# Performance work log

Hardware: AMD Instinct MI355X
Metric: run time of the kernel (lower is better)

## Reference

```python
import jax, jax.numpy as jnp
import numpy as np

# Scaled-down LLaMA-style decoder with per-layer memory K/V prefix (tokenmix2 Decoder)
L, D, H, Dh, F, V = 2, 4096, 32, 128, 8192, 8192
B, S, M = 1, 1024, 512
EPS = 1e-5
ROPE_BASE = 10000.0


def setup_inputs() -> dict:
    key = jax.random.key(0)
    ks = jax.random.split(key, 16)
    sd = D ** -0.5
    sf = F ** -0.5
    n = lambda k, shape, s: (jax.random.normal(k, shape, jnp.float32) * s)
    return {
        "input_ids": jax.random.randint(ks[0], (B, S), 0, V),
        "memory": jax.random.normal(ks[1], (L, B, M, D), jnp.float32),
        "embed": n(ks[2], (V, D), sd),
        "Wq": n(ks[3], (L, D, D), sd),
        "Wk": n(ks[4], (L, D, D), sd),
        "Wv": n(ks[5], (L, D, D), sd),
        "Wo": n(ks[6], (L, D, D), sd),
        "Wg": n(ks[7], (L, F, D), sd),
        "Wu": n(ks[8], (L, F, D), sd),
        "Wd": n(ks[9], (L, D, F), sf),
        "Wmk": n(ks[10], (L, D, D), sd),
        "Wmv": n(ks[11], (L, D, D), sd),
        "ln1": jnp.ones((L, D), jnp.float32),
        "ln2": jnp.ones((L, D), jnp.float32),
        "normw": jnp.ones((D,), jnp.float32),
        "lm_head": n(ks[12], (V, D), sd),
    }


def _rms(x, w):
    return x * jax.lax.rsqrt(jnp.mean(x * x, axis=-1, keepdims=True) + EPS) * w


def _rot_half(x):
    x1, x2 = jnp.split(x, 2, axis=-1)
    return jnp.concatenate([-x2, x1], axis=-1)


def _rope_tables(n_pos):
    inv_freq = 1.0 / (ROPE_BASE ** (jnp.arange(0, Dh, 2, dtype=jnp.float32) / Dh))
    ang = jnp.arange(n_pos, dtype=jnp.float32)[:, None] * inv_freq[None, :]
    emb = jnp.concatenate([ang, ang], axis=-1)  # [n_pos, Dh]
    return jnp.cos(emb), jnp.sin(emb)


def reference(input_ids, memory, embed, Wq, Wk, Wv, Wo, Wg, Wu, Wd, Wmk, Wmv,
              ln1, ln2, normw, lm_head):
    h = embed[input_ids]                                   # [B,S,D]
    cos, sin = _rope_tables(M + S)                         # memory tokens sit at positions 0..M
    cos_k, sin_k = cos[None, None], sin[None, None]        # [1,1,M+S,Dh]
    cos_q, sin_q = cos[None, None, M:], sin[None, None, M:]  # queries at positions M..M+S
    qpos = jnp.arange(M, M + S)
    kpos = jnp.arange(M + S)
    mask = qpos[:, None] >= kpos[None, :]                  # causal incl. full memory prefix
    scale = Dh ** -0.5

    def heads(x, T):
        return x.reshape(B, T, H, Dh).transpose(0, 2, 1, 3)  # [B,H,T,Dh]

    for l in range(L):
        x = _rms(h, ln1[l])
        q = heads(x @ Wq[l].T, S)
        k = heads(x @ Wk[l].T, S)
        v = heads(x @ Wv[l].T, S)
        mk = heads(memory[l] @ Wmk[l].T, M)
        mv = heads(memory[l] @ Wmv[l].T, M)
        K = jnp.concatenate([mk, k], axis=2)               # [B,H,M+S,Dh]
        Vv = jnp.concatenate([mv, v], axis=2)
        q = q * cos_q + _rot_half(q) * sin_q
        K = K * cos_k + _rot_half(K) * sin_k
        scores = jnp.einsum('bhqd,bhkd->bhqk', q, K) * scale
        scores = jnp.where(mask, scores, jnp.float32(-1e30))
        p = jax.nn.softmax(scores, axis=-1)
        o = jnp.einsum('bhqk,bhkd->bhqd', p, Vv)
        o = o.transpose(0, 2, 1, 3).reshape(B, S, D)
        h = h + o @ Wo[l].T
        x = _rms(h, ln2[l])
        h = h + (jax.nn.silu(x @ Wg[l].T) * (x @ Wu[l].T)) @ Wd[l].T

    h = _rms(h, normw)
    logits = (h @ lm_head.T).astype(jnp.float32)           # [B,S,V]
    return logits
```

## Files before the change

kernel.cpp:

```cpp
#include <hip/hip_runtime.h>
#include <hip/hip_bf16.h>

typedef unsigned int uint;
typedef unsigned short u16;

#define D_ 4096
#define H_ 32
#define DH 128
#define F_ 8192
#define V_ 8192
#define S_ 1024
#define M_ 512
#define L_ 2
#define KV_ (M_ + S_)

typedef __attribute__((ext_vector_type(8))) short s16x8;
typedef __attribute__((ext_vector_type(4))) float f32x4;
typedef __attribute__((ext_vector_type(4))) u16 u16x4;

__device__ __forceinline__ u16 f2bf(float f) {
    uint u = __float_as_uint(f);
    u += 0x7FFFu + ((u >> 16) & 1u);
    return (u16)(u >> 16);
}
__device__ __forceinline__ float bf2f(u16 h) {
    return __uint_as_float(((uint)h) << 16);
}
__device__ __forceinline__ void gload_lds16(const void* g, void* l) {
    __builtin_amdgcn_global_load_lds(
        (const __attribute__((address_space(1))) unsigned int*)g,
        (__attribute__((address_space(3))) unsigned int*)l, 16, 0, 0);
}

__global__ void k_embed(const int* __restrict__ ids, const float* __restrict__ embed,
                        float* __restrict__ h) {
    int row = blockIdx.x;
    const float4* src = (const float4*)(embed + (size_t)ids[row] * D_);
    float4* dst = (float4*)(h + (size_t)row * D_);
    for (int i = threadIdx.x; i < D_ / 4; i += 256) dst[i] = src[i];
}

__global__ __launch_bounds__(256) void k_rms(const float* __restrict__ hin,
                                             const float* __restrict__ w,
                                             u16* __restrict__ out) {
    int row = blockIdx.x, t = threadIdx.x;
    const float4* src = (const float4*)(hin + (size_t)row * D_);
    float4 v[4];
    float ss = 0.f;
#pragma unroll
    for (int i = 0; i < 4; ++i) {
        v[i] = src[t + 256 * i];
        ss += v[i].x * v[i].x + v[i].y * v[i].y + v[i].z * v[i].z + v[i].w * v[i].w;
    }
#pragma unroll
    for (int off = 32; off; off >>= 1) ss += __shfl_xor(ss, off);
    __shared__ float red[4];
    if ((t & 63) == 0) red[t >> 6] = ss;
    __syncthreads();
    float tot = red[0] + red[1] + red[2] + red[3];
    float sc = rsqrtf(tot * (1.0f / D_) + 1e-5f);
    const float4* wp = (const float4*)w;
    u16x4* op = (u16x4*)(out + (size_t)row * D_);
#pragma unroll
    for (int i = 0; i < 4; ++i) {
        float4 wv = wp[t + 256 * i];
        u16x4 o;
        o[0] = f2bf(v[i].x * sc * wv.x);
        o[1] = f2bf(v[i].y * sc * wv.y);
        o[2] = f2bf(v[i].z * sc * wv.z);
        o[3] = f2bf(v[i].w * sc * wv.w);
        op[t + 256 * i] = o;
    }
}

__global__ void k_cvt(const float* __restrict__ src, u16* __restrict__ dst, int n4) {
    int i = blockIdx.x * 256 + threadIdx.x;
    if (i < n4) {
        float4 v = ((const float4*)src)[i];
        u16x4 o;
        o[0] = f2bf(v.x); o[1] = f2bf(v.y); o[2] = f2bf(v.z); o[3] = f2bf(v.w);
        ((u16x4*)dst)[i] = o;
    }
}

__global__ void k_silu(const float* __restrict__ G, const float* __restrict__ U,
                       u16* __restrict__ out, int n4) {
    int i = blockIdx.x * 256 + threadIdx.x;
    if (i < n4) {
        float4 g = ((const float4*)G)[i];
        float4 u = ((const float4*)U)[i];
        u16x4 o;
        o[0] = f2bf(g.x / (1.0f + __expf(-g.x)) * u.x);
        o[1] = f2bf(g.y / (1.0f + __expf(-g.y)) * u.y);
        o[2] = f2bf(g.z / (1.0f + __expf(-g.z)) * u.z);
        o[3] = f2bf(g.w / (1.0f + __expf(-g.w)) * u.w);
        ((u16x4*)out)[i] = o;
    }
}

__global__ void k_ropetab(float* __restrict__ tab) {
    int pos = blockIdx.x, i = threadIdx.x;
    float invf = powf(10000.0f, -(float)i * (1.0f / 64.0f));
    float ang = (float)pos * invf;
    tab[(size_t)pos * 128 + i * 2] = cosf(ang);
    tab[(size_t)pos * 128 + i * 2 + 1] = sinf(ang);
}

__global__ __launch_bounds__(256) void k_rope(u16* __restrict__ buf,
                                              const float* __restrict__ tab, int pos0) {
    int row = blockIdx.x, t = threadIdx.x;
    const float2* tp = (const float2*)(tab + (size_t)(pos0 + row) * 128);
    u16* p = buf + (size_t)row * D_;
#pragma unroll
    for (int j = 0; j < 8; ++j) {
        int pid = t + 256 * j;
        int hd = pid >> 6, i = pid & 63;
        float2 cs = tp[i];
        int base = hd * 128 + i;
        float v0 = bf2f(p[base]), v1 = bf2f(p[base + 64]);
        p[base] = f2bf(v0 * cs.x - v1 * cs.y);
        p[base + 64] = f2bf(v1 * cs.x + v0 * cs.y);
    }
}

__global__ __launch_bounds__(256) void k_transpose(const u16* __restrict__ src,
                                                   u16* __restrict__ dst) {
    __shared__ u16 tile[64][66];
    int tc = blockIdx.x * 64;
    int tr = blockIdx.y * 64;
    int t = threadIdx.x;
    int c = t & 63, r0 = t >> 6;
#pragma unroll
    for (int i = 0; i < 16; ++i) {
        int r = r0 + i * 4;
        tile[r][c] = src[(size_t)(tr + r) * D_ + tc + c];
    }
    __syncthreads();
#pragma unroll
    for (int i = 0; i < 16; ++i) {
        int r = r0 + i * 4;
        dst[(size_t)(tc + r) * KV_ + tr + c] = tile[c][r];
    }
}

struct GemmB8 {
    const u16* A[5];
    const u16* B[5];
    void* O[5];
    int mrows[5];
};

template <int EPI>
__global__ __launch_bounds__(512, 2) void k_gemm8(GemmB8 P, int Nn, int Kfull) {
    int z = blockIdx.z;
    size_t bm = blockIdx.y, bn = blockIdx.x;
    if ((int)(bm * 256) >= P.mrows[z]) return;
    const u16* A = P.A[z];
    const u16* Bw = P.B[z];
    __shared__ __align__(16) u16 AB[2][2][2][128][64];

    const int tid = threadIdx.x;
    const int lane = tid & 63, wid = tid >> 6;
    const int l16 = lane & 15, lh = lane >> 4;
    const int wrow = (wid >> 2) * 64;
    const int wcol = (wid & 3) * 32;
    const int nt = Kfull >> 6;

    const int grow0 = tid >> 3;
    const int gsw = ((tid & 7) ^ (grow0 & 7)) * 8;
    const u16* pA = A + (size_t)(bm * 256 + grow0) * Kfull + gsw;
    const u16* pB = Bw + (size_t)(bn * 256 + grow0) * Kfull + gsw;

    auto stage = [&](const u16* base, int mat, int h, int t) {
        if (t >= nt) return;
        const u16* g = base + (size_t)(h * 128) * Kfull + t * 64;
        u16* l = &AB[t & 1][mat][h][0][0] + tid * 8;
        gload_lds16(g, l);
        gload_lds16(g + (size_t)64 * Kfull, l + 4096);
    };

    f32x4 acc[4][4][2];
#pragma unroll
    for (int q = 0; q < 4; ++q)
#pragma unroll
        for (int mf = 0; mf < 4; ++mf)
#pragma unroll
            for (int nf = 0; nf < 2; ++nf)
#pragma unroll
                for (int e = 0; e < 4; ++e) acc[q][mf][nf][e] = 0.f;

    stage(pA, 0, 0, 0); stage(pB, 1, 0, 0);
    stage(pA, 0, 1, 0); stage(pB, 1, 1, 0);
    stage(pA, 0, 0, 1); stage(pB, 1, 0, 1);
    asm volatile("s_waitcnt vmcnt(4)" ::: "memory");
    __builtin_amdgcn_s_barrier();
    asm volatile("" ::: "memory");

    for (int T = 0; T < nt; ++T) {
        const int cb = T & 1;
#pragma unroll
        for (int q = 0; q < 4; ++q) {
            const int qm = q >> 1, qn = q & 1;
            s16x8 af[4][2], bb[2][2];
#pragma unroll
            for (int kk = 0; kk < 2; ++kk) {
                const int g0 = kk * 4 + lh;
                const int sw = (g0 ^ (l16 & 7)) * 8;
#pragma unroll
                for (int mf = 0; mf < 4; ++mf)
                    af[mf][kk] = *(const s16x8*)(&AB[cb][0][qm][wrow + mf * 16 + l16][sw]);
#pragma unroll
                for (int nf = 0; nf < 2; ++nf)
                    bb[nf][kk] = *(const s16x8*)(&AB[cb][1][qn][wcol + nf * 16 + l16][sw]);
            }
            if (q == 0) stage(pA, 0, 1, T + 1);
            else if (q == 1) stage(pB, 1, 1, T + 1);
            else if (q == 2) stage(pA, 0, 0, T + 2);
            else stage(pB, 1, 0, T + 2);
            asm volatile("" ::: "memory");
            __builtin_amdgcn_s_barrier();
            asm volatile("" ::: "memory");
            __builtin_amdgcn_s_setprio(1);
#pragma unroll
            for (int kk = 0; kk < 2; ++kk)
#pragma unroll
                for (int mf = 0; mf < 4; ++mf)
#pragma unroll
                    for (int nf = 0; nf < 2; ++nf)
                        acc[q][mf][nf] = __builtin_amdgcn_mfma_f32_16x16x32_bf16(
                            af[mf][kk], bb[nf][kk], acc[q][mf][nf], 0, 0, 0);
            __builtin_amdgcn_s_setprio(0);
            if (q == 3) {
                if (T < nt - 2) asm volatile("s_waitcnt vmcnt(4)" ::: "memory");
                else if (T == nt - 2) asm volatile("s_waitcnt vmcnt(0)" ::: "memory");
            }
            asm volatile("" ::: "memory");
            __builtin_amdgcn_s_barrier();
            asm volatile("" ::: "memory");
        }
    }

    void* Oo = P.O[z];
#pragma unroll
    for (int q = 0; q < 4; ++q) {
        const int qm = q >> 1, qn = q & 1;
#pragma unroll
        for (int mf = 0; mf < 4; ++mf) {
#pragma unroll
            for (int nf = 0; nf < 2; ++nf) {
#pragma unroll
                for (int rr = 0; rr < 4; ++rr) {
                    int grow = (int)bm * 256 + qm * 128 + wrow + mf * 16 + lh * 4 + rr;
                    int gcol = (int)bn * 256 + qn * 128 + wcol + nf * 16 + l16;
                    size_t idx = (size_t)grow * Nn + gcol;
                    float v = acc[q][mf][nf][rr];
                    if constexpr (EPI == 0) ((u16*)Oo)[idx] = f2bf(v);
                    else ((float*)Oo)[idx] = v;
                }
            }
        }
    }
}

struct GemmB2 {
    const u16* A[5];
    const u16* B[5];
    void* O[5];
    int mrows[5];
};

template <int EPI>
__global__ __launch_bounds__(256) void k_gemm2(GemmB2 P, int Nn, int Kfull) {
    int z = blockIdx.z;
    size_t bm = blockIdx.y, bn = blockIdx.x;
    if ((int)(bm * 128) >= P.mrows[z]) return;
    const u16* A = P.A[z];
    const u16* Bw = P.B[z];
    __shared__ __align__(16) u16 As[128 * 64];
    __shared__ __align__(16) u16 Bs[128 * 64];
    int tid = threadIdx.x;
    int lane = tid & 63, wid = tid >> 6;
    int l16 = lane & 15, lh = lane >> 4;
    int wm = (wid >> 1) * 64, wn = (wid & 1) * 64;

    const u16 *pA[4], *pB[4];
    int ldso[4];
#pragma unroll
    for (int i = 0; i < 4; ++i) {
        int c = tid + 256 * i;
        int r = c >> 3, s = c & 7;
        int ssw = (s ^ (r & 7)) * 8;
        pA[i] = A + (size_t)(bm * 128 + r) * Kfull + ssw;
        pB[i] = Bw + (size_t)(bn * 128 + r) * Kfull + ssw;
        ldso[i] = c * 8;
    }

    f32x4 acc[4][4];
#pragma unroll
    for (int i = 0; i < 4; ++i)
#pragma unroll
        for (int j = 0; j < 4; ++j)
#pragma unroll
            for (int e = 0; e < 4; ++e) acc[i][j][e] = 0.f;

    int nt = Kfull >> 6;
    for (int t = 0; t < nt; ++t) {
        int k0 = t << 6;
#pragma unroll
        for (int i = 0; i < 4; ++i) gload_lds16(pA[i] + k0, &As[ldso[i]]);
#pragma unroll
        for (int i = 0; i < 4; ++i) gload_lds16(pB[i] + k0, &Bs[ldso[i]]);
        __syncthreads();
#pragma unroll
        for (int kk = 0; kk < 2; ++kk) {
            int sidx = kk * 4 + lh;
            int sw = (sidx ^ (l16 & 7)) * 8;
            s16x8 af[4], bf4[4];
#pragma unroll
            for (int mi = 0; mi < 4; ++mi)
                af[mi] = *(const s16x8*)(&As[(wm + mi * 16 + l16) * 64 + sw]);
#pragma unroll
            for (int ni = 0; ni < 4; ++ni)
                bf4[ni] = *(const s16x8*)(&Bs[(wn + ni * 16 + l16) * 64 + sw]);
#pragma unroll
            for (int mi = 0; mi < 4; ++mi)
#pragma unroll
                for (int ni = 0; ni < 4; ++ni)
                    acc[mi][ni] = __builtin_amdgcn_mfma_f32_16x16x32_bf16(
                        af[mi], bf4[ni], acc[mi][ni], 0, 0, 0);
        }
        __syncthreads();
    }

    void* Oo = P.O[z];
#pragma unroll
    for (int mi = 0; mi < 4; ++mi) {
#pragma unroll
        for (int ni = 0; ni < 4; ++ni) {
#pragma unroll
            for (int r = 0; r < 4; ++r) {
                int grow = (int)bm * 128 + wm + mi * 16 + lh * 4 + r;
                int gcol = (int)bn * 128 + wn + ni * 16 + l16;
                size_t idx = (size_t)grow * Nn + gcol;
                float v = acc[mi][ni][r];
                if constexpr (EPI == 1) ((float*)Oo)[idx] = v;
                else ((float*)Oo)[idx] += v;
            }
        }
    }
}

__global__ __launch_bounds__(64) void k_attn(const u16* __restrict__ Qb,
                                             const u16* __restrict__ Kb,
                                             const u16* __restrict__ VT,
                                             u16* __restrict__ Ob) {
    int qt = blockIdx.x, hd = blockIdx.y;
    int lane = threadIdx.x, l16 = lane & 15, lh = lane >> 4;
    __shared__ __align__(16) float Pl[16 * 36];

    s16x8 qf[4];
#pragma unroll
    for (int c = 0; c < 4; ++c)
        qf[c] = *(const s16x8*)(Qb + (size_t)(qt * 16 + l16) * D_ + hd * DH + c * 32 + lh * 8);

    f32x4 o[8];
#pragma unroll
    for (int dc = 0; dc < 8; ++dc)
#pragma unroll
        for (int e = 0; e < 4; ++e) o[dc][e] = 0.f;
    float m[4], lsum[4];
#pragma unroll
    for (int r = 0; r < 4; ++r) { m[r] = -1e30f; lsum[r] = 0.f; }

    const float scale = 0.08838834764831845f;
    int qbase = M_ + qt * 16;
    int nkb = (M_ + qt * 16 + 16 + 31) >> 5;

    for (int kb = 0; kb < nkb; ++kb) {
        f32x4 s0, s1;
#pragma unroll
        for (int e = 0; e < 4; ++e) { s0[e] = 0.f; s1[e] = 0.f; }
#pragma unroll
        for (int c = 0; c < 4; ++c) {
            s16x8 kf0 = *(const s16x8*)(Kb + (size_t)(kb * 32 + l16) * D_ + hd * DH + c * 32 + lh * 8);
            s16x8 kf1 = *(const s16x8*)(Kb + (size_t)(kb * 32 + 16 + l16) * D_ + hd * DH + c * 32 + lh * 8);
            s0 = __builtin_amdgcn_mfma_f32_16x16x32_bf16(qf[c], kf0, s0, 0, 0, 0);
            s1 = __builtin_amdgcn_mfma_f32_16x16x32_bf16(qf[c], kf1, s1, 0, 0, 0);
        }
        int kp0 = kb * 32 + l16, kp1 = kp0 + 16;
        float pm[4];
#pragma unroll
        for (int r = 0; r < 4; ++r) {
            int qp = qbase + lh * 4 + r;
            float v0 = s0[r] * scale; if (kp0 > qp) v0 = -1e30f;
            float v1 = s1[r] * scale; if (kp1 > qp) v1 = -1e30f;
            s0[r] = v0; s1[r] = v1;
            pm[r] = fmaxf(v0, v1);
        }
#pragma unroll
        for (int r = 0; r < 4; ++r) {
#pragma unroll
            for (int off = 8; off; off >>= 1) pm[r] = fmaxf(pm[r], __shfl_xor(pm[r], off));
        }
        float alpha[4];
#pragma unroll
        for (int r = 0; r < 4; ++r) {
            float mn = fmaxf(m[r], pm[r]);
            alpha[r] = __expf(m[r] - mn);
            m[r] = mn;
            float p0 = __expf(s0[r] - mn), p1 = __expf(s1[r] - mn);
            s0[r] = p0; s1[r] = p1;
            float t = p0 + p1;
#pragma unroll
            for (int off = 8; off; off >>= 1) t += __shfl_xor(t, off);
            lsum[r] = lsum[r] * alpha[r] + t;
        }
#pragma unroll
        for (int r = 0; r < 4; ++r) {
            Pl[(lh * 4 + r) * 36 + l16] = s0[r];
            Pl[(lh * 4 + r) * 36 + 16 + l16] = s1[r];
        }
        __syncthreads();
        s16x8 pf;
        {
            const f32x4* pp = (const f32x4*)(Pl + l16 * 36 + lh * 8);
            f32x4 a = pp[0], b = pp[1];
            pf[0] = (short)f2bf(a[0]); pf[1] = (short)f2bf(a[1]);
            pf[2] = (short)f2bf(a[2]); pf[3] = (short)f2bf(a[3]);
            pf[4] = (short)f2bf(b[0]); pf[5] = (short)f2bf(b[1]);
            pf[6] = (short)f2bf(b[2]); pf[7] = (short)f2bf(b[3]);
        }
        __syncthreads();
#pragma unroll
        for (int dc = 0; dc < 8; ++dc) {
#pragma unroll
            for (int r = 0; r < 4; ++r) o[dc][r] *= alpha[r];
        }
#pragma unroll
        for (int dc = 0; dc < 8; ++dc) {
            s16x8 vf = *(const s16x8*)(VT + (size_t)(hd * DH + dc * 16 + l16) * KV_ + kb * 32 + lh * 8);
            o[dc] = __builtin_amdgcn_mfma_f32_16x16x32_bf16(pf, vf, o[dc], 0, 0, 0);
        }
    }
#pragma unroll
    for (int dc = 0; dc < 8; ++dc) {
#pragma unroll
        for (int r = 0; r < 4; ++r) {
            float val = o[dc][r] / lsum[r];
            Ob[(size_t)(qt * 16 + lh * 4 + r) * D_ + hd * DH + dc * 16 + l16] = f2bf(val);
        }
    }
}

extern "C" void kernel_launch(void* const* d_in, const int* in_sizes, int n_in,
                              void* d_out, int out_size, void* d_ws, size_t ws_size,
                              hipStream_t stream) {
    const int* ids = (const int*)d_in[0];
    const float* memory = (const float*)d_in[1];
    const float* embed = (const float*)d_in[2];
    const float* Wq = (const float*)d_in[3];
    const float* Wk = (const float*)d_in[4];
    const float* Wv = (const float*)d_in[5];
    const float* Wo = (const float*)d_in[6];
    const float* Wg = (const float*)d_in[7];
    const float* Wu = (const float*)d_in[8];
    const float* Wd = (const float*)d_in[9];
    const float* Wmk = (const float*)d_in[10];
    const float* Wmv = (const float*)d_in[11];
    const float* ln1 = (const float*)d_in[12];
    const float* ln2 = (const float*)d_in[13];
    const float* normw = (const float*)d_in[14];
    const float* lm = (const float*)d_in[15];

    char* ws = (char*)d_ws;
    float* h   = (float*)(ws + 0x0000000);
    u16* xb    = (u16*)(ws + 0x1000000);
    float* tab = (float*)(ws + 0x1800000);
    u16* memb  = (u16*)(ws + 0x1900000);
    u16* Qb    = (u16*)(ws + 0x1E00000);
    u16* Kb    = (u16*)(ws + 0x2600000);
    u16* Vb    = (u16*)(ws + 0x3200000);
    u16* VT    = (u16*)(ws + 0x3E00000);
    u16* Ob    = (u16*)(ws + 0x4A00000);
    float* Gbuf = (float*)(ws + 0x1E00000);
    u16* tb     = (u16*)(ws + 0x3E00000);
    float* Ubuf = (float*)(ws + 0x4E00000);
    u16* Wqb  = (u16*)(ws + 0x07000000);
    u16* Wkb  = (u16*)(ws + 0x0B000000);
    u16* Wvb  = (u16*)(ws + 0x0F000000);
    u16* Wob  = (u16*)(ws + 0x13000000);
    u16* Wmkb = (u16*)(ws + 0x17000000);
    u16* Wmvb = (u16*)(ws + 0x1B000000);
    u16* Wgb  = (u16*)(ws + 0x1F000000);
    u16* Wub  = (u16*)(ws + 0x27000000);
    u16* Wdb  = (u16*)(ws + 0x2F000000);
    u16* lmb  = (u16*)(ws + 0x37000000);

    const int nDD = L_ * D_ * D_ / 4, nFD = L_ * F_ * D_ / 4, nVD = V_ * D_ / 4;
    k_cvt<<<(nDD + 255) / 256, 256, 0, stream>>>(Wq, Wqb, nDD);
    k_cvt<<<(nDD + 255) / 256, 256, 0, stream>>>(Wk, Wkb, nDD);
    k_cvt<<<(nDD + 255) / 256, 256, 0, stream>>>(Wv, Wvb, nDD);
    k_cvt<<<(nDD + 255) / 256, 256, 0, stream>>>(Wo, Wob, nDD);
    k_cvt<<<(nDD + 255) / 256, 256, 0, stream>>>(Wmk, Wmkb, nDD);
    k_cvt<<<(nDD + 255) / 256, 256, 0, stream>>>(Wmv, Wmvb, nDD);
    k_cvt<<<(nFD + 255) / 256, 256, 0, stream>>>(Wg, Wgb, nFD);
    k_cvt<<<(nFD + 255) / 256, 256, 0, stream>>>(Wu, Wub, nFD);
    k_cvt<<<(nFD + 255) / 256, 256, 0, stream>>>(Wd, Wdb, nFD);
    k_cvt<<<(nVD + 255) / 256, 256, 0, stream>>>(lm, lmb, nVD);

    k_embed<<<S_, 256, 0, stream>>>(ids, embed, h);
    k_ropetab<<<KV_, 64, 0, stream>>>(tab);

    for (int l = 0; l < L_; ++l) {
        const size_t oDD = (size_t)l * D_ * D_;
        const size_t oFD = (size_t)l * F_ * D_;

        k_rms<<<S_, 256, 0, stream>>>(h, ln1 + l * D_, xb);
        k_cvt<<<(M_ * D_ / 4 + 255) / 256, 256, 0, stream>>>(
            memory + (size_t)l * M_ * D_, memb, M_ * D_ / 4);

        GemmB8 g1{};
        g1.A[0] = xb;   g1.B[0] = Wqb + oDD;  g1.O[0] = Qb;                    g1.mrows[0] = S_;
        g1.A[1] = xb;   g1.B[1] = Wkb + oDD;  g1.O[1] = Kb + (size_t)M_ * D_;  g1.mrows[1] = S_;
        g1.A[2] = xb;   g1.B[2] = Wvb + oDD;  g1.O[2] = Vb + (size_t)M_ * D_;  g1.mrows[2] = S_;
        g1.A[3] = memb; g1.B[3] = Wmkb + oDD; g1.O[3] = Kb;                    g1.mrows[3] = M_;
        g1.A[4] = memb; g1.B[4] = Wmvb + oDD; g1.O[4] = Vb;                    g1.mrows[4] = M_;
        k_gemm8<0><<<dim3(D_ / 256, S_ / 256, 5), 512, 0, stream>>>(g1, D_, D_);

        k_rope<<<S_, 256, 0, stream>>>(Qb, tab, M_);
        k_rope<<<KV_, 256, 0, stream>>>(Kb, tab, 0);
        k_transpose<<<dim3(D_ / 64, KV_ / 64), 256, 0, stream>>>(Vb, VT);
        k_attn<<<dim3(S_ / 16, H_), 64, 0, stream>>>(Qb, Kb, VT, Ob);

        GemmB2 g2{};
        g2.A[0] = Ob; g2.B[0] = Wob + oDD; g2.O[0] = h; g2.mrows[0] = S_;
        k_gemm2<2><<<dim3(D_ / 128, S_ / 128, 1), 256, 0, stream>>>(g2, D_, D_);

        k_rms<<<S_, 256, 0, stream>>>(h, ln2 + l * D_, xb);
        GemmB8 g3{};
        g3.A[0] = xb; g3.B[0] = Wgb + oFD; g3.O[0] = Gbuf; g3.mrows[0] = S_;
        g3.A[1] = xb; g3.B[1] = Wub + oFD; g3.O[1] = Ubuf; g3.mrows[1] = S_;
        k_gemm8<1><<<dim3(F_ / 256, S_ / 256, 2), 512, 0, stream>>>(g3, F_, D_);
        k_silu<<<(S_ * F_ / 4 + 255) / 256, 256, 0, stream>>>(Gbuf, Ubuf, tb, S_ * F_ / 4);
        GemmB2 g5{};
        g5.A[0] = tb; g5.B[0] = Wdb + oFD; g5.O[0] = h; g5.mrows[0] = S_;
        k_gemm2<2><<<dim3(D_ / 128, S_ / 128, 1), 256, 0, stream>>>(g5, D_, F_);
    }

    k_rms<<<S_, 256, 0, stream>>>(h, normw, xb);
    GemmB2 g6{};
    g6.A[0] = xb; g6.B[0] = lmb; g6.O[0] = (float*)d_out; g6.mrows[0] = S_;
    k_gemm2<1><<<dim3(V_ / 128, S_ / 128, 1), 256, 0, stream>>>(g6, V_, D_);
}
```

Measured before the change: 2.155 ms.

## Fuse fp32-to-bf16 weight conversion into GEMM B-operand loading

Drops the separate conversion kernels that turned every fp32 weight matrix into bf16 in the workspace before each run. The GEMM kernels now read fp32 weights directly into registers, convert them with packed bf16 instructions and write them swizzled into LDS, with the prefetch schedule and wait counts reworked. This removes a full read and write pass over roughly a gigabyte of weights. In exchange the GEMMs read twice the bytes for B, and register-staged loads replace the asynchronous direct-to-LDS path, which can hurt latency hiding. Gate and up GEMM tiles are reused across 4 row blocks, so they re-read fp32 several times.

After: 1.955 ms. 9.3% less time.

```diff
diff --git a/kernel.cpp b/kernel.cpp
--- a/kernel.cpp
+++ b/kernel.cpp
@@ -25,6 +25,11 @@
 }
 __device__ __forceinline__ float bf2f(u16 h) {
     return __uint_as_float(((uint)h) << 16);
+}
+__device__ __forceinline__ uint cvt_pk_bf16(float a, float b) {
+    uint r;
+    asm volatile("v_cvt_pk_bf16_f32 %0, %1, %2" : "=v"(r) : "v"(a), "v"(b));
+    return r;
 }
 __device__ __forceinline__ void gload_lds16(const void* g, void* l) {
     __builtin_amdgcn_global_load_lds(
@@ -145,7 +150,7 @@
 
 struct GemmB8 {
     const u16* A[5];
-    const u16* B[5];
+    const float* B[5];
     void* O[5];
     int mrows[5];
 };
@@ -156,7 +161,7 @@
     size_t bm = blockIdx.y, bn = blockIdx.x;
     if ((int)(bm * 256) >= P.mrows[z]) return;
     const u16* A = P.A[z];
-    const u16* Bw = P.B[z];
+    const float* Bw = P.B[z];
     __shared__ __align__(16) u16 AB[2][2][2][128][64];
 
     const int tid = threadIdx.x;
@@ -169,16 +174,38 @@
     const int grow0 = tid >> 3;
     const int gsw = ((tid & 7) ^ (grow0 & 7)) * 8;
     const u16* pA = A + (size_t)(bm * 256 + grow0) * Kfull + gsw;
-    const u16* pB = Bw + (size_t)(bn * 256 + grow0) * Kfull + gsw;
-
-    auto stage = [&](const u16* base, int mat, int h, int t) {
+    auto stageA = [&](int h, int t) {
         if (t >= nt) return;
-        const u16* g = base + (size_t)(h * 128) * Kfull + t * 64;
-        u16* l = &AB[t & 1][mat][h][0][0] + tid * 8;
+        const u16* g = pA + (size_t)(h * 128) * Kfull + t * 64;
+        u16* l = &AB[t & 1][0][h][0][0] + tid * 8;
         gload_lds16(g, l);
         gload_lds16(g + (size_t)64 * Kfull, l + 4096);
     };
 
+    const int brow = tid >> 3;
+    const int bg = tid & 7;
+    const float* pB = Bw + (size_t)(bn * 256 + brow) * Kfull + bg * 8;
+    const int bwo = ((bg ^ (brow & 7)) * 8);
+    auto loadB = [&](int h, int t, float4* br) {
+        if (t >= nt) return;
+        const float* g = pB + (size_t)(h * 128) * Kfull + t * 64;
+        br[0] = *(const float4*)g;
+        br[1] = *(const float4*)(g + 4);
+        const float* g2 = g + (size_t)64 * Kfull;
+        br[2] = *(const float4*)g2;
+        br[3] = *(const float4*)(g2 + 4);
+    };
+    auto writeB = [&](int h, int t, const float4* br) {
+        if (t >= nt) return;
+        uint4 w0, w1;
+        w0.x = cvt_pk_bf16(br[0].x, br[0].y); w0.y = cvt_pk_bf16(br[0].z, br[0].w);
+        w0.z = cvt_pk_bf16(br[1].x, br[1].y); w0.w = cvt_pk_bf16(br[1].z, br[1].w);
+        w1.x = cvt_pk_bf16(br[2].x, br[2].y); w1.y = cvt_pk_bf16(br[2].z, br[2].w);
+        w1.z = cvt_pk_bf16(br[3].x, br[3].y); w1.w = cvt_pk_bf16(br[3].z, br[3].w);
+        *(uint4*)(&AB[t & 1][1][h][brow][bwo]) = w0;
+        *(uint4*)(&AB[t & 1][1][h][brow + 64][bwo]) = w1;
+    };
+
     f32x4 acc[4][4][2];
 #pragma unroll
     for (int q = 0; q < 4; ++q)
@@ -189,10 +216,15 @@
 #pragma unroll
                 for (int e = 0; e < 4; ++e) acc[q][mf][nf][e] = 0.f;
 
-    stage(pA, 0, 0, 0); stage(pB, 1, 0, 0);
-    stage(pA, 0, 1, 0); stage(pB, 1, 1, 0);
-    stage(pA, 0, 0, 1); stage(pB, 1, 0, 1);
-    asm volatile("s_waitcnt vmcnt(4)" ::: "memory");
+    float4 brE[4], brO[4];
+    stageA(0, 0); stageA(1, 0); stageA(0, 1);
+    {
+        float4 b0[4], b1[4], b2[4];
+        loadB(0, 0, b0); loadB(1, 0, b1); loadB(0, 1, b2);
+        writeB(0, 0, b0); writeB(1, 0, b1); writeB(0, 1, b2);
+        loadB(1, 1, brO);
+    }
+    asm volatile("s_waitcnt lgkmcnt(0)" ::: "memory");
     __builtin_amdgcn_s_barrier();
     asm volatile("" ::: "memory");
 
@@ -213,10 +245,19 @@
                 for (int nf = 0; nf < 2; ++nf)
                     bb[nf][kk] = *(const s16x8*)(&AB[cb][1][qn][wcol + nf * 16 + l16][sw]);
             }
-            if (q == 0) stage(pA, 0, 1, T + 1);
-            else if (q == 1) stage(pB, 1, 1, T + 1);
-            else if (q == 2) stage(pA, 0, 0, T + 2);
-            else stage(pB, 1, 0, T + 2);
+            if (q == 0) {
+                loadB(0, T + 2, brE);
+            } else if (q == 1) {
+                writeB(1, T + 1, brO);
+                stageA(1, T + 1);
+                asm volatile("s_waitcnt lgkmcnt(0)" ::: "memory");
+            } else if (q == 2) {
+                loadB(1, T + 2, brO);
+            } else {
+                writeB(0, T + 2, brE);
+                stageA(0, T + 2);
+                asm volatile("s_waitcnt lgkmcnt(0)" ::: "memory");
+            }
             asm volatile("" ::: "memory");
             __builtin_amdgcn_s_barrier();
             asm volatile("" ::: "memory");
@@ -231,8 +272,8 @@
                             af[mf][kk], bb[nf][kk], acc[q][mf][nf], 0, 0, 0);
             __builtin_amdgcn_s_setprio(0);
             if (q == 3) {
-                if (T < nt - 2) asm volatile("s_waitcnt vmcnt(4)" ::: "memory");
-                else if (T == nt - 2) asm volatile("s_waitcnt vmcnt(0)" ::: "memory");
+                if (T < nt - 3) asm volatile("s_waitcnt vmcnt(6)" ::: "memory");
+                else asm volatile("s_waitcnt vmcnt(0)" ::: "memory");
             }
             asm volatile("" ::: "memory");
             __builtin_amdgcn_s_barrier();
@@ -264,7 +305,7 @@
 
 struct GemmB2 {
     const u16* A[5];
-    const u16* B[5];
+    const float* B[5];
     void* O[5];
     int mrows[5];
 };
@@ -275,7 +316,7 @@
     size_t bm = blockIdx.y, bn = blockIdx.x;
     if ((int)(bm * 128) >= P.mrows[z]) return;
     const u16* A = P.A[z];
-    const u16* Bw = P.B[z];
+    const float* Bw = P.B[z];
     __shared__ __align__(16) u16 As[128 * 64];
     __shared__ __align__(16) u16 Bs[128 * 64];
     int tid = threadIdx.x;
@@ -283,16 +324,17 @@
     int l16 = lane & 15, lh = lane >> 4;
     int wm = (wid >> 1) * 64, wn = (wid & 1) * 64;
 
-    const u16 *pA[4], *pB[4];
-    int ldso[4];
+    const u16* pA[4];
+    const float* pB[4];
+    int ldso[4], bso[4];
 #pragma unroll
     for (int i = 0; i < 4; ++i) {
         int c = tid + 256 * i;
         int r = c >> 3, s = c & 7;
-        int ssw = (s ^ (r & 7)) * 8;
-        pA[i] = A + (size_t)(bm * 128 + r) * Kfull + ssw;
-        pB[i] = Bw + (size_t)(bn * 128 + r) * Kfull + ssw;
+        pA[i] = A + (size_t)(bm * 128 + r) * Kfull + ((s ^ (r & 7)) * 8);
+        pB[i] = Bw + (size_t)(bn * 128 + r) * Kfull + s * 8;
         ldso[i] = c * 8;
+        bso[i] = r * 64 + ((s ^ (r & 7)) * 8);
     }
 
     f32x4 acc[4][4];
@@ -303,13 +345,34 @@
 #pragma unroll
             for (int e = 0; e < 4; ++e) acc[i][j][e] = 0.f;
 
+    float4 br[8];
+    auto loadB = [&](int k0) {
+#pragma unroll
+        for (int i = 0; i < 4; ++i) {
+            br[2 * i] = *(const float4*)(pB[i] + k0);
+            br[2 * i + 1] = *(const float4*)(pB[i] + k0 + 4);
+        }
+    };
+    auto cvtwriteB = [&]() {
+#pragma unroll
+        for (int i = 0; i < 4; ++i) {
+            uint4 w;
+            w.x = cvt_pk_bf16(br[2 * i].x, br[2 * i].y);
+            w.y = cvt_pk_bf16(br[2 * i].z, br[2 * i].w);
+            w.z = cvt_pk_bf16(br[2 * i + 1].x, br[2 * i + 1].y);
+            w.w = cvt_pk_bf16(br[2 * i + 1].z, br[2 * i + 1].w);
+            *(uint4*)(&Bs[bso[i]]) = w;
+        }
+    };
+
     int nt = Kfull >> 6;
+    loadB(0);
     for (int t = 0; t < nt; ++t) {
-        int k0 = t << 6;
-#pragma unroll
-        for (int i = 0; i < 4; ++i) gload_lds16(pA[i] + k0, &As[ldso[i]]);
-#pragma unroll
-        for (int i = 0; i < 4; ++i) gload_lds16(pB[i] + k0, &Bs[ldso[i]]);
+#pragma unroll
+        for (int i = 0; i < 4; ++i) gload_lds16(pA[i] + (t << 6), &As[ldso[i]]);
+        cvtwriteB();
+        if (t + 1 < nt) loadB((t + 1) << 6);
+        asm volatile("s_waitcnt vmcnt(8) lgkmcnt(0)" ::: "memory");
         __syncthreads();
 #pragma unroll
         for (int kk = 0; kk < 2; ++kk) {
@@ -485,28 +548,6 @@
     float* Gbuf = (float*)(ws + 0x1E00000);
     u16* tb     = (u16*)(ws + 0x3E00000);
     float* Ubuf = (float*)(ws + 0x4E00000);
-    u16* Wqb  = (u16*)(ws + 0x07000000);
-    u16* Wkb  = (u16*)(ws + 0x0B000000);
-    u16* Wvb  = (u16*)(ws + 0x0F000000);
-    u16* Wob  = (u16*)(ws + 0x13000000);
-    u16* Wmkb = (u16*)(ws + 0x17000000);
-    u16* Wmvb = (u16*)(ws + 0x1B000000);
-    u16* Wgb  = (u16*)(ws + 0x1F000000);
-    u16* Wub  = (u16*)(ws + 0x27000000);
-    u16* Wdb  = (u16*)(ws + 0x2F000000);
-    u16* lmb  = (u16*)(ws + 0x37000000);
-
-    const int nDD = L_ * D_ * D_ / 4, nFD = L_ * F_ * D_ / 4, nVD = V_ * D_ / 4;
-    k_cvt<<<(nDD + 255) / 256, 256, 0, stream>>>(Wq, Wqb, nDD);
-    k_cvt<<<(nDD + 255) / 256, 256, 0, stream>>>(Wk, Wkb, nDD);
-    k_cvt<<<(nDD + 255) / 256, 256, 0, stream>>>(Wv, Wvb, nDD);
-    k_cvt<<<(nDD + 255) / 256, 256, 0, stream>>>(Wo, Wob, nDD);
-    k_cvt<<<(nDD + 255) / 256, 256, 0, stream>>>(Wmk, Wmkb, nDD);
-    k_cvt<<<(nDD + 255) / 256, 256, 0, stream>>>(Wmv, Wmvb, nDD);
-    k_cvt<<<(nFD + 255) / 256, 256, 0, stream>>>(Wg, Wgb, nFD);
-    k_cvt<<<(nFD + 255) / 256, 256, 0, stream>>>(Wu, Wub, nFD);
-    k_cvt<<<(nFD + 255) / 256, 256, 0, stream>>>(Wd, Wdb, nFD);
-    k_cvt<<<(nVD + 255) / 256, 256, 0, stream>>>(lm, lmb, nVD);
 
     k_embed<<<S_, 256, 0, stream>>>(ids, embed, h);
     k_ropetab<<<KV_, 64, 0, stream>>>(tab);
@@ -520,11 +561,11 @@
             memory + (size_t)l * M_ * D_, memb, M_ * D_ / 4);
 
         GemmB8 g1{};
-        g1.A[0] = xb;   g1.B[0] = Wqb + oDD;  g1.O[0] = Qb;                    g1.mrows[0] = S_;
-        g1.A[1] = xb;   g1.B[1] = Wkb + oDD;  g1.O[1] = Kb + (size_t)M_ * D_;  g1.mrows[1] = S_;
-        g1.A[2] = xb;   g1.B[2] = Wvb + oDD;  g1.O[2] = Vb + (size_t)M_ * D_;  g1.mrows[2] = S_;
-        g1.A[3] = memb; g1.B[3] = Wmkb + oDD; g1.O[3] = Kb;                    g1.mrows[3] = M_;
-        g1.A[4] = memb; g1.B[4] = Wmvb + oDD; g1.O[4] = Vb;                    g1.mrows[4] = M_;
+        g1.A[0] = xb;   g1.B[0] = Wq + oDD;  g1.O[0] = Qb;                    g1.mrows[0] = S_;
+        g1.A[1] = xb;   g1.B[1] = Wk + oDD;  g1.O[1] = Kb + (size_t)M_ * D_;  g1.mrows[1] = S_;
+        g1.A[2] = xb;   g1.B[2] = Wv + oDD;  g1.O[2] = Vb + (size_t)M_ * D_;  g1.mrows[2] = S_;
+        g1.A[3] = memb; g1.B[3] = Wmk + oDD; g1.O[3] = Kb;                    g1.mrows[3] = M_;
+        g1.A[4] = memb; g1.B[4] = Wmv + oDD; g1.O[4] = Vb;                    g1.mrows[4] = M_;
         k_gemm8<0><<<dim3(D_ / 256, S_ / 256, 5), 512, 0, stream>>>(g1, D_, D_);
 
         k_rope<<<S_, 256, 0, stream>>>(Qb, tab, M_);
@@ -533,22 +574,22 @@
         k_attn<<<dim3(S_ / 16, H_), 64, 0, stream>>>(Qb, Kb, VT, Ob);
 
         GemmB2 g2{};
-        g2.A[0] = Ob; g2.B[0] = Wob + oDD; g2.O[0] = h; g2.mrows[0] = S_;
+        g2.A[0] = Ob; g2.B[0] = Wo + oDD; g2.O[0] = h; g2.mrows[0] = S_;
         k_gemm2<2><<<dim3(D_ / 128, S_ / 128, 1), 256, 0, stream>>>(g2, D_, D_);
 
         k_rms<<<S_, 256, 0, stream>>>(h, ln2 + l * D_, xb);
         GemmB8 g3{};
-        g3.A[0] = xb; g3.B[0] = Wgb + oFD; g3.O[0] = Gbuf; g3.mrows[0] = S_;
-        g3.A[1] = xb; g3.B[1] = Wub + oFD; g3.O[1] = Ubuf; g3.mrows[1] = S_;
+        g3.A[0] = xb; g3.B[0] = Wg + oFD; g3.O[0] = Gbuf; g3.mrows[0] = S_;
+        g3.A[1] = xb; g3.B[1] = Wu + oFD; g3.O[1] = Ubuf; g3.mrows[1] = S_;
         k_gemm8<1><<<dim3(F_ / 256, S_ / 256, 2), 512, 0, stream>>>(g3, F_, D_);
         k_silu<<<(S_ * F_ / 4 + 255) / 256, 256, 0, stream>>>(Gbuf, Ubuf, tb, S_ * F_ / 4);
         GemmB2 g5{};
-        g5.A[0] = tb; g5.B[0] = Wdb + oFD; g5.O[0] = h; g5.mrows[0] = S_;
+        g5.A[0] = tb; g5.B[0] = Wd + oFD; g5.O[0] = h; g5.mrows[0] = S_;
         k_gemm2<2><<<dim3(D_ / 128, S_ / 128, 1), 256, 0, stream>>>(g5, D_, F_);
     }
 
     k_rms<<<S_, 256, 0, stream>>>(h, normw, xb);
     GemmB2 g6{};
-    g6.A[0] = xb; g6.B[0] = lmb; g6.O[0] = (float*)d_out; g6.mrows[0] = S_;
+    g6.A[0] = xb; g6.B[0] = lm; g6.O[0] = (float*)d_out; g6.mrows[0] = S_;
     k_gemm2<1><<<dim3(V_ / 128, S_ / 128, 1), 256, 0, stream>>>(g6, V_, D_);
 }
```

## Split-K residual GEMMs with atomics, bf16 gate/up outputs, reuse A fragments in gemm8

Applied to the files above, without the earlier changes.

The Wo and down-projection GEMMs are split along K into two halves dispatched via blockIdx.z, and each half accumulates into the fp32 residual with atomicAdd. This doubles the number of blocks on grids that had only 256 tiles. The gate/up GEMM now writes bf16 instead of fp32, which halves the intermediate traffic, and the SiLU kernel reads bf16 eight values at a time. The gemm8 main loop is manually unrolled so A fragments are reused across quadrants instead of reloaded. Split-K adds atomic traffic and makes the summation order nondeterministic, and rounding gate/up to bf16 before SiLU adds some error.

Measured after the change: 1.885 ms. -12.5%, faster.

```diff
diff --git a/kernel.cpp b/kernel.cpp
--- a/kernel.cpp
+++ b/kernel.cpp
@@ -83,18 +83,19 @@
     }
 }
 
-__global__ void k_silu(const float* __restrict__ G, const float* __restrict__ U,
-                       u16* __restrict__ out, int n4) {
+__global__ void k_silu(const u16* __restrict__ G, const u16* __restrict__ U,
+                       u16* __restrict__ out, int n8) {
     int i = blockIdx.x * 256 + threadIdx.x;
-    if (i < n4) {
-        float4 g = ((const float4*)G)[i];
-        float4 u = ((const float4*)U)[i];
-        u16x4 o;
-        o[0] = f2bf(g.x / (1.0f + __expf(-g.x)) * u.x);
-        o[1] = f2bf(g.y / (1.0f + __expf(-g.y)) * u.y);
-        o[2] = f2bf(g.z / (1.0f + __expf(-g.z)) * u.z);
-        o[3] = f2bf(g.w / (1.0f + __expf(-g.w)) * u.w);
-        ((u16x4*)out)[i] = o;
+    if (i < n8) {
+        s16x8 g = ((const s16x8*)G)[i];
+        s16x8 u = ((const s16x8*)U)[i];
+        s16x8 o;
+#pragma unroll
+        for (int j = 0; j < 8; ++j) {
+            float gv = bf2f((u16)g[j]), uv = bf2f((u16)u[j]);
+            o[j] = (short)f2bf(gv / (1.0f + __expf(-gv)) * uv);
+        }
+        ((s16x8*)out)[i] = o;
     }
 }
 
@@ -198,46 +199,115 @@
 
     for (int T = 0; T < nt; ++T) {
         const int cb = T & 1;
-#pragma unroll
-        for (int q = 0; q < 4; ++q) {
-            const int qm = q >> 1, qn = q & 1;
-            s16x8 af[4][2], bb[2][2];
-#pragma unroll
-            for (int kk = 0; kk < 2; ++kk) {
-                const int g0 = kk * 4 + lh;
-                const int sw = (g0 ^ (l16 & 7)) * 8;
-#pragma unroll
-                for (int mf = 0; mf < 4; ++mf)
-                    af[mf][kk] = *(const s16x8*)(&AB[cb][0][qm][wrow + mf * 16 + l16][sw]);
+        s16x8 af[4][2], bb[2][2];
+
+#pragma unroll
+        for (int kk = 0; kk < 2; ++kk) {
+            const int sw = ((kk * 4 + lh) ^ (l16 & 7)) * 8;
+#pragma unroll
+            for (int mf = 0; mf < 4; ++mf)
+                af[mf][kk] = *(const s16x8*)(&AB[cb][0][0][wrow + mf * 16 + l16][sw]);
+#pragma unroll
+            for (int nf = 0; nf < 2; ++nf)
+                bb[nf][kk] = *(const s16x8*)(&AB[cb][1][0][wcol + nf * 16 + l16][sw]);
+        }
+        stage(pA, 0, 1, T + 1);
+        asm volatile("" ::: "memory");
+        __builtin_amdgcn_s_barrier();
+        asm volatile("" ::: "memory");
+        __builtin_amdgcn_s_setprio(1);
+#pragma unroll
+        for (int kk = 0; kk < 2; ++kk)
+#pragma unroll
+            for (int mf = 0; mf < 4; ++mf)
 #pragma unroll
                 for (int nf = 0; nf < 2; ++nf)
-                    bb[nf][kk] = *(const s16x8*)(&AB[cb][1][qn][wcol + nf * 16 + l16][sw]);
-            }
-            if (q == 0) stage(pA, 0, 1, T + 1);
-            else if (q == 1) stage(pB, 1, 1, T + 1);
-            else if (q == 2) stage(pA, 0, 0, T + 2);
-            else stage(pB, 1, 0, T + 2);
-            asm volatile("" ::: "memory");
-            __builtin_amdgcn_s_barrier();
-            asm volatile("" ::: "memory");
-            __builtin_amdgcn_s_setprio(1);
-#pragma unroll
-            for (int kk = 0; kk < 2; ++kk)
-#pragma unroll
-                for (int mf = 0; mf < 4; ++mf)
-#pragma unroll
-                    for (int nf = 0; nf < 2; ++nf)
-                        acc[q][mf][nf] = __builtin_amdgcn_mfma_f32_16x16x32_bf16(
-                            af[mf][kk], bb[nf][kk], acc[q][mf][nf], 0, 0, 0);
-            __builtin_amdgcn_s_setprio(0);
-            if (q == 3) {
-                if (T < nt - 2) asm volatile("s_waitcnt vmcnt(4)" ::: "memory");
-                else if (T == nt - 2) asm volatile("s_waitcnt vmcnt(0)" ::: "memory");
-            }
-            asm volatile("" ::: "memory");
-            __builtin_amdgcn_s_barrier();
-            asm volatile("" ::: "memory");
-        }
+                    acc[0][mf][nf] = __builtin_amdgcn_mfma_f32_16x16x32_bf16(
+                        af[mf][kk], bb[nf][kk], acc[0][mf][nf], 0, 0, 0);
+        __builtin_amdgcn_s_setprio(0);
+        asm volatile("" ::: "memory");
+        __builtin_amdgcn_s_barrier();
+        asm volatile("" ::: "memory");
+
+#pragma unroll
+        for (int kk = 0; kk < 2; ++kk) {
+            const int sw = ((kk * 4 + lh) ^ (l16 & 7)) * 8;
+#pragma unroll
+            for (int nf = 0; nf < 2; ++nf)
+                bb[nf][kk] = *(const s16x8*)(&AB[cb][1][1][wcol + nf * 16 + l16][sw]);
+        }
+        stage(pB, 1, 1, T + 1);
+        asm volatile("" ::: "memory");
+        __builtin_amdgcn_s_barrier();
+        asm volatile("" ::: "memory");
+        __builtin_amdgcn_s_setprio(1);
+#pragma unroll
+        for (int kk = 0; kk < 2; ++kk)
+#pragma unroll
+            for (int mf = 0; mf < 4; ++mf)
+#pragma unroll
+                for (int nf = 0; nf < 2; ++nf)
+                    acc[1][mf][nf] = __builtin_amdgcn_mfma_f32_16x16x32_bf16(
+                        af[mf][kk], bb[nf][kk], acc[1][mf][nf], 0, 0, 0);
+        __builtin_amdgcn_s_setprio(0);
+        asm volatile("" ::: "memory");
+        __builtin_amdgcn_s_barrier();
+        asm volatile("" ::: "memory");
+
+#pragma unroll
+        for (int kk = 0; kk < 2; ++kk) {
+            const int sw = ((kk * 4 + lh) ^ (l16 & 7)) * 8;
+#pragma unroll
+            for (int mf = 0; mf < 4; ++mf)
+                af[mf][kk] = *(const s16x8*)(&AB[cb][0][1][wrow + mf * 16 + l16][sw]);
+#pragma unroll
+            for (int nf = 0; nf < 2; ++nf)
+                bb[nf][kk] = *(const s16x8*)(&AB[cb][1][0][wcol + nf * 16 + l16][sw]);
+        }
+        stage(pA, 0, 0, T + 2);
+        asm volatile("" ::: "memory");
+        __builtin_amdgcn_s_barrier();
+        asm volatile("" ::: "memory");
+        __builtin_amdgcn_s_setprio(1);
+#pragma unroll
+        for (int kk = 0; kk < 2; ++kk)
+#pragma unroll
+            for (int mf = 0; mf < 4; ++mf)
+#pragma unroll
+                for (int nf = 0; nf < 2; ++nf)
+                    acc[2][mf][nf] = __builtin_amdgcn_mfma_f32_16x16x32_bf16(
+                        af[mf][kk], bb[nf][kk], acc[2][mf][nf], 0, 0, 0);
+        __builtin_amdgcn_s_setprio(0);
+        asm volatile("" ::: "memory");
+        __builtin_amdgcn_s_barrier();
+        asm volatile("" ::: "memory");
+
+#pragma unroll
+        for (int kk = 0; kk < 2; ++kk) {
+            const int sw = ((kk * 4 + lh) ^ (l16 & 7)) * 8;
+#pragma unroll
+            for (int nf = 0; nf < 2; ++nf)
+                bb[nf][kk] = *(const s16x8*)(&AB[cb][1][1][wcol + nf * 16 + l16][sw]);
+        }
+        stage(pB, 1, 0, T + 2);
+        asm volatile("" ::: "memory");
+        __builtin_amdgcn_s_barrier();
+        asm volatile("" ::: "memory");
+        __builtin_amdgcn_s_setprio(1);
+#pragma unroll
+        for (int kk = 0; kk < 2; ++kk)
+#pragma unroll
+            for (int mf = 0; mf < 4; ++mf)
+#pragma unroll
+                for (int nf = 0; nf < 2; ++nf)
+                    acc[3][mf][nf] = __builtin_amdgcn_mfma_f32_16x16x32_bf16(
+                        af[mf][kk], bb[nf][kk], acc[3][mf][nf], 0, 0, 0);
+        __builtin_amdgcn_s_setprio(0);
+        if (T < nt - 2) asm volatile("s_waitcnt vmcnt(4)" ::: "memory");
+        else if (T == nt - 2) asm volatile("s_waitcnt vmcnt(0)" ::: "memory");
+        asm volatile("" ::: "memory");
+        __builtin_amdgcn_s_barrier();
+        asm volatile("" ::: "memory");
     }
 
     void* Oo = P.O[z];
@@ -267,15 +337,17 @@
     const u16* B[5];
     void* O[5];
     int mrows[5];
+    int koff[5];
 };
 
 template <int EPI>
-__global__ __launch_bounds__(256) void k_gemm2(GemmB2 P, int Nn, int Kfull) {
+__global__ __launch_bounds__(256) void k_gemm2(GemmB2 P, int Nn, int Kstep, int Kfull) {
     int z = blockIdx.z;
     size_t bm = blockIdx.y, bn = blockIdx.x;
     if ((int)(bm * 128) >= P.mrows[z]) return;
     const u16* A = P.A[z];
     const u16* Bw = P.B[z];
+    int koff = P.koff[z];
     __shared__ __align__(16) u16 As[128 * 64];
     __shared__ __align__(16) u16 Bs[128 * 64];
     int tid = threadIdx.x;
@@ -290,8 +362,8 @@
         int c = tid + 256 * i;
         int r = c >> 3, s = c & 7;
         int ssw = (s ^ (r & 7)) * 8;
-        pA[i] = A + (size_t)(bm * 128 + r) * Kfull + ssw;
-        pB[i] = Bw + (size_t)(bn * 128 + r) * Kfull + ssw;
+        pA[i] = A + (size_t)(bm * 128 + r) * Kfull + koff + ssw;
+        pB[i] = Bw + (size_t)(bn * 128 + r) * Kfull + koff + ssw;
         ldso[i] = c * 8;
     }
 
@@ -303,7 +375,7 @@
 #pragma unroll
             for (int e = 0; e < 4; ++e) acc[i][j][e] = 0.f;
 
-    int nt = Kfull >> 6;
+    int nt = Kstep >> 6;
     for (int t = 0; t < nt; ++t) {
         int k0 = t << 6;
 #pragma unroll
@@ -344,7 +416,7 @@
                 size_t idx = (size_t)grow * Nn + gcol;
                 float v = acc[mi][ni][r];
                 if constexpr (EPI == 1) ((float*)Oo)[idx] = v;
-                else ((float*)Oo)[idx] += v;
+                else atomicAdd((float*)Oo + idx, v);
             }
         }
     }
@@ -482,9 +554,9 @@
     u16* Vb    = (u16*)(ws + 0x3200000);
     u16* VT    = (u16*)(ws + 0x3E00000);
     u16* Ob    = (u16*)(ws + 0x4A00000);
-    float* Gbuf = (float*)(ws + 0x1E00000);
-    u16* tb     = (u16*)(ws + 0x3E00000);
-    float* Ubuf = (float*)(ws + 0x4E00000);
+    u16* Gb16  = (u16*)(ws + 0x1E00000);
+    u16* Ub16  = (u16*)(ws + 0x2E00000);
+    u16* tb    = (u16*)(ws + 0x3E00000);
     u16* Wqb  = (u16*)(ws + 0x07000000);
     u16* Wkb  = (u16*)(ws + 0x0B000000);
     u16* Wvb  = (u16*)(ws + 0x0F000000);
@@ -533,22 +605,24 @@
         k_attn<<<dim3(S_ / 16, H_), 64, 0, stream>>>(Qb, Kb, VT, Ob);
 
         GemmB2 g2{};
-        g2.A[0] = Ob; g2.B[0] = Wob + oDD; g2.O[0] = h; g2.mrows[0] = S_;
-        k_gemm2<2><<<dim3(D_ / 128, S_ / 128, 1), 256, 0, stream>>>(g2, D_, D_);
+        g2.A[0] = Ob; g2.B[0] = Wob + oDD; g2.O[0] = h; g2.mrows[0] = S_; g2.koff[0] = 0;
+        g2.A[1] = Ob; g2.B[1] = Wob + oDD; g2.O[1] = h; g2.mrows[1] = S_; g2.koff[1] = 2048;
+        k_gemm2<4><<<dim3(D_ / 128, S_ / 128, 2), 256, 0, stream>>>(g2, D_, 2048, D_);
 
         k_rms<<<S_, 256, 0, stream>>>(h, ln2 + l * D_, xb);
         GemmB8 g3{};
-        g3.A[0] = xb; g3.B[0] = Wgb + oFD; g3.O[0] = Gbuf; g3.mrows[0] = S_;
-        g3.A[1] = xb; g3.B[1] = Wub + oFD; g3.O[1] = Ubuf; g3.mrows[1] = S_;
-        k_gemm8<1><<<dim3(F_ / 256, S_ / 256, 2), 512, 0, stream>>>(g3, F_, D_);
-        k_silu<<<(S_ * F_ / 4 + 255) / 256, 256, 0, stream>>>(Gbuf, Ubuf, tb, S_ * F_ / 4);
+        g3.A[0] = xb; g3.B[0] = Wgb + oFD; g3.O[0] = Gb16; g3.mrows[0] = S_;
+        g3.A[1] = xb; g3.B[1] = Wub + oFD; g3.O[1] = Ub16; g3.mrows[1] = S_;
+        k_gemm8<0><<<dim3(F_ / 256, S_ / 256, 2), 512, 0, stream>>>(g3, F_, D_);
+        k_silu<<<(S_ * F_ / 8 + 255) / 256, 256, 0, stream>>>(Gb16, Ub16, tb, S_ * F_ / 8);
         GemmB2 g5{};
-        g5.A[0] = tb; g5.B[0] = Wdb + oFD; g5.O[0] = h; g5.mrows[0] = S_;
-        k_gemm2<2><<<dim3(D_ / 128, S_ / 128, 1), 256, 0, stream>>>(g5, D_, F_);
+        g5.A[0] = tb; g5.B[0] = Wdb + oFD; g5.O[0] = h; g5.mrows[0] = S_; g5.koff[0] = 0;
+        g5.A[1] = tb; g5.B[1] = Wdb + oFD; g5.O[1] = h; g5.mrows[1] = S_; g5.koff[1] = 4096;
+        k_gemm2<4><<<dim3(D_ / 128, S_ / 128, 2), 256, 0, stream>>>(g5, D_, 4096, F_);
     }
 
     k_rms<<<S_, 256, 0, stream>>>(h, normw, xb);
     GemmB2 g6{};
-    g6.A[0] = xb; g6.B[0] = lmb; g6.O[0] = (float*)d_out; g6.mrows[0] = S_;
-    k_gemm2<1><<<dim3(V_ / 128, S_ / 128, 1), 256, 0, stream>>>(g6, V_, D_);
-}
+    g6.A[0] = xb; g6.B[0] = lmb; g6.O[0] = (float*)d_out; g6.mrows[0] = S_; g6.koff[0] = 0;
+    k_gemm2<1><<<dim3(V_ / 128, S_ / 128, 1), 256, 0, stream>>>(g6, V_, D_, D_);
+}
```
